# Kernel optimization log

Hardware: AMD Instinct MI355X
Metric: run time of the kernel (lower is better)

Reference implementation:

```python
import jax, jax.numpy as jnp
import numpy as np

B, S, E = 4, 4096, 512

def setup_inputs() -> dict:
    key = jax.random.key(0)
    ks = jax.random.split(key, 9)
    scale = 1.0 / np.sqrt(E)  # keep linear weights at realistic init scale
    return {
        "query": jax.random.normal(ks[0], (B, S, E), jnp.float32),
        "key":   jax.random.normal(ks[1], (B, S, E), jnp.float32),
        "value": jax.random.normal(ks[2], (B, S, E), jnp.float32),
        "Wq": jax.random.normal(ks[3], (E, E), jnp.float32) * scale,
        "bq": jax.random.normal(ks[4], (E,), jnp.float32) * scale,
        "Wk": jax.random.normal(ks[5], (E, E), jnp.float32) * scale,
        "bk": jax.random.normal(ks[6], (E,), jnp.float32) * scale,
        "Wv": jax.random.normal(ks[7], (E, E), jnp.float32) * scale,
        "bv": jax.random.normal(ks[8], (E,), jnp.float32) * scale,
    }

def reference(query, key, value, Wq, bq, Wk, bk, Wv, bv):
    # torch Linear: x @ W^T + b
    q = jnp.einsum('bse,oe->bso', query, Wq) + bq
    k = jnp.einsum('bse,oe->bso', key,   Wk) + bk
    v = jnp.einsum('bse,oe->bso', value, Wv) + bv
    # NOTE: module applies NO 1/sqrt(d) scaling (faithful to source)
    scores = jnp.einsum('bqd,bkd->bqk', q, k)          # [B,S,S] materialized
    attn = jax.nn.softmax(scores, axis=-1)
    # dropout is identity in eval / for deterministic reference
    return jnp.einsum('bqk,bkd->bqd', attn, v)         # [B,S,E]
```

## Files before the change

### kernel.cpp

```cpp
#include <hip/hip_runtime.h>

typedef __attribute__((ext_vector_type(8))) _Float16 f16x8;
typedef __attribute__((ext_vector_type(4))) _Float16 f16x4;
typedef __attribute__((ext_vector_type(4))) float f32x4;

#define NB 4
#define NS 4096
#define NE 512

__device__ __forceinline__ f16x8 cvt2(float4 a, float4 b) {
    f16x8 r;
    r[0] = (_Float16)a.x; r[1] = (_Float16)a.y; r[2] = (_Float16)a.z; r[3] = (_Float16)a.w;
    r[4] = (_Float16)b.x; r[5] = (_Float16)b.y; r[6] = (_Float16)b.z; r[7] = (_Float16)b.w;
    return r;
}
__device__ __forceinline__ void gload_lds16(const void* g, void* l) {
    __builtin_amdgcn_global_load_lds(
        (const __attribute__((address_space(1))) void*)g,
        (__attribute__((address_space(3))) void*)l, 16, 0, 0);
}

__global__ __launch_bounds__(256) void proj_kernel(
    const float* __restrict__ Xq, const float* __restrict__ Xk,
    const float* __restrict__ Xv,
    const float* __restrict__ Wq, const float* __restrict__ Wk,
    const float* __restrict__ Wv,
    const float* __restrict__ bq, const float* __restrict__ bk,
    const float* __restrict__ bv,
    _Float16* __restrict__ oq, _Float16* __restrict__ ok,
    _Float16* __restrict__ ovt, int b0)
{
    __shared__ __align__(16) _Float16 As[128 * 32];
    __shared__ __align__(16) _Float16 Bs[128 * 32];
    const int t = threadIdx.x;
    const int w = t >> 6, ln = t & 63;
    const int which = blockIdx.y;
    const float* X    = (which == 0) ? Xq : ((which == 1) ? Xk : Xv);
    const float* W    = (which == 0) ? Wq : ((which == 1) ? Wk : Wv);
    const float* bias = (which == 0) ? bq : ((which == 1) ? bk : bv);

    const int m0 = (blockIdx.x >> 2) * 128;
    const int n0 = (blockIdx.x & 3) * 128;

    const int srow  = t >> 1;
    const int shalf = (t & 1) * 16;
    const float* gA = X + ((size_t)b0 * NS + m0 + srow) * NE + shalf;
    const float* gB = W + (size_t)(n0 + srow) * NE + shalf;
    _Float16* lA = &As[srow * 32 + shalf];
    _Float16* lB = &Bs[srow * 32 + shalf];

    f32x4 acc[4][4] = {};
    const int wm = (w >> 1) * 64, wn = (w & 1) * 64;
    const int lcol = ln & 15, lq = ln >> 4;

    for (int k0 = 0; k0 < NE; k0 += 32) {
        float4 xa0 = *(const float4*)(gA + k0);
        float4 xa1 = *(const float4*)(gA + k0 + 4);
        float4 xa2 = *(const float4*)(gA + k0 + 8);
        float4 xa3 = *(const float4*)(gA + k0 + 12);
        float4 xb0 = *(const float4*)(gB + k0);
        float4 xb1 = *(const float4*)(gB + k0 + 4);
        float4 xb2 = *(const float4*)(gB + k0 + 8);
        float4 xb3 = *(const float4*)(gB + k0 + 12);
        __syncthreads();
        *(f16x8*)lA       = cvt2(xa0, xa1);
        *(f16x8*)(lA + 8) = cvt2(xa2, xa3);
        *(f16x8*)lB       = cvt2(xb0, xb1);
        *(f16x8*)(lB + 8) = cvt2(xb2, xb3);
        __syncthreads();
        f16x8 a[4], b[4];
#pragma unroll
        for (int i = 0; i < 4; i++)
            a[i] = *(const f16x8*)&As[(wm + i * 16 + lcol) * 32 + lq * 8];
#pragma unroll
        for (int j = 0; j < 4; j++)
            b[j] = *(const f16x8*)&Bs[(wn + j * 16 + lcol) * 32 + lq * 8];
#pragma unroll
        for (int i = 0; i < 4; i++)
#pragma unroll
            for (int j = 0; j < 4; j++)
                acc[i][j] = __builtin_amdgcn_mfma_f32_16x16x32_f16(a[i], b[j], acc[i][j], 0, 0, 0);
    }

    if (which == 0) {
#pragma unroll
        for (int j = 0; j < 4; j++) {
            const int col = n0 + wn + j * 16 + lcol;
            const float bb = bias[col];
#pragma unroll
            for (int i = 0; i < 4; i++) {
                const int rbase = m0 + wm + i * 16 + lq * 4;
#pragma unroll
                for (int r = 0; r < 4; r++)
                    oq[(size_t)(rbase + r) * NE + col] = (_Float16)(acc[i][j][r] + bb);
            }
        }
    } else if (which == 1) {
#pragma unroll
        for (int j = 0; j < 4; j++) {
            const int col = n0 + wn + j * 16 + lcol;
            const int cch = col >> 3, clo = col & 7;
            const float bb = bias[col];
#pragma unroll
            for (int i = 0; i < 4; i++) {
                const int rbase = m0 + wm + i * 16 + lq * 4;
#pragma unroll
                for (int r = 0; r < 4; r++) {
                    const int s = rbase + r;
                    ok[(size_t)s * NE + ((cch ^ (s & 7)) << 3) + clo] =
                        (_Float16)(acc[i][j][r] + bb);
                }
            }
        }
    } else {
#pragma unroll
        for (int j = 0; j < 4; j++) {
            const int d = n0 + wn + j * 16 + lcol;
            const float bb = bias[d];
#pragma unroll
            for (int i = 0; i < 4; i++) {
                const int rbase = m0 + wm + i * 16 + lq * 4;
                const int bat = rbase >> 12;
                const int sl  = rbase & 4095;
                const int kc  = sl >> 6;
                const int slot = ((sl >> 3) & 7) ^ (d & 7);
                f16x4 pk;
#pragma unroll
                for (int r = 0; r < 4; r++) pk[r] = (_Float16)(acc[i][j][r] + bb);
                *(f16x4*)&ovt[(((size_t)bat * 64 + kc) * NE + d) * 64 + slot * 8 + (sl & 7)] = pk;
            }
        }
    }
}

__global__ __launch_bounds__(512, 2) void attn_kernel(
    const _Float16* __restrict__ q, const _Float16* __restrict__ ksw,
    const _Float16* __restrict__ vsw, float* __restrict__ out, int b0)
{
    __shared__ __align__(16) _Float16 Kbuf[64 * 512];
    __shared__ __align__(16) _Float16 Vbuf[512 * 64];
    __shared__ __align__(16) _Float16 Pb[64 * 72];
    __shared__ float mpart[2][64];
    __shared__ float lpart[2][64];

    const int t = threadIdx.x, w = t >> 6, ln = t & 63;
    const int lcol = ln & 15, lq = ln >> 4;
    const int rt = w & 3, g = w >> 2;
    const int xm = lcol & 7;
    const int rel = blockIdx.y, babs = b0 + rel;
    const int q0 = blockIdx.x * 64;

    const _Float16* qp = q + ((size_t)rel * NS + q0 + rt * 16 + lcol) * NE + lq * 8;
    f16x8 qf[16];
#pragma unroll
    for (int ks = 0; ks < 16; ks++) qf[ks] = *(const f16x8*)(qp + ks * 32);

    const _Float16* kbase = ksw + (size_t)rel * NS * NE;
    const _Float16* vbase = vsw + (size_t)rel * NS * NE;

    f32x4 oacc[16] = {};
    float m_st[4] = {-1e30f, -1e30f, -1e30f, -1e30f};
    float l_st[4] = {0.f, 0.f, 0.f, 0.f};

    for (int kc = 0; kc < 64; kc++) {
        __syncthreads();
        const _Float16* kc_src = kbase + (size_t)kc * 64 * NE;
        const _Float16* vc_src = vbase + (size_t)kc * NE * 64;
#pragma unroll
        for (int i = 0; i < 8; i++) {
            const int blk = i * 8 + w;
            gload_lds16(kc_src + (size_t)blk * 512 + ln * 8, (_Float16*)Kbuf + blk * 512);
            gload_lds16(vc_src + (size_t)blk * 512 + ln * 8, (_Float16*)Vbuf + blk * 512);
        }
        __syncthreads();

        f32x4 s0 = {}, s1 = {};
#pragma unroll
        for (int ks = 0; ks < 16; ks++) {
            const int ch = ((ks * 4 + lq) ^ xm) * 8;
            f16x8 kb0 = *(const f16x8*)&Kbuf[(g * 32 + lcol) * 512 + ch];
            f16x8 kb1 = *(const f16x8*)&Kbuf[(g * 32 + 16 + lcol) * 512 + ch];
            s0 = __builtin_amdgcn_mfma_f32_16x16x32_f16(qf[ks], kb0, s0, 0, 0, 0);
            s1 = __builtin_amdgcn_mfma_f32_16x16x32_f16(qf[ks], kb1, s1, 0, 0, 0);
        }
#pragma unroll
        for (int r = 0; r < 4; r++) {
            float vmx = fmaxf(s0[r], s1[r]);
#pragma unroll
            for (int msk = 8; msk; msk >>= 1) vmx = fmaxf(vmx, __shfl_xor(vmx, msk, 64));
            if (lcol == 0) mpart[g][rt * 16 + lq * 4 + r] = vmx;
        }
        __syncthreads();

        float alpha[4];
#pragma unroll
        for (int r = 0; r < 4; r++) {
            const int row = rt * 16 + lq * 4 + r;
            float mc = fmaxf(mpart[0][row], mpart[1][row]);
            float mn = fmaxf(m_st[r], mc);
            alpha[r] = __expf(m_st[r] - mn);
            float p0 = __expf(s0[r] - mn);
            float p1 = __expf(s1[r] - mn);
            Pb[row * 72 + g * 32 + lcol]      = (_Float16)p0;
            Pb[row * 72 + g * 32 + 16 + lcol] = (_Float16)p1;
            float sm = p0 + p1;
#pragma unroll
            for (int msk = 8; msk; msk >>= 1) sm += __shfl_xor(sm, msk, 64);
            if (lcol == 0) lpart[g][row] = sm;
            m_st[r] = mn;
        }
        __syncthreads();
#pragma unroll
        for (int r = 0; r < 4; r++) {
            const int row = rt * 16 + lq * 4 + r;
            l_st[r] = l_st[r] * alpha[r] + lpart[0][row] + lpart[1][row];
        }
        bool allone = (alpha[0] == 1.f) & (alpha[1] == 1.f) &
                      (alpha[2] == 1.f) & (alpha[3] == 1.f);
        if (!__all(allone)) {
#pragma unroll
            for (int et = 0; et < 16; et++) {
                oacc[et][0] *= alpha[0]; oacc[et][1] *= alpha[1];
                oacc[et][2] *= alpha[2]; oacc[et][3] *= alpha[3];
            }
        }
        f16x8 pa0 = *(const f16x8*)&Pb[(rt * 16 + lcol) * 72 + lq * 8];
        f16x8 pa1 = *(const f16x8*)&Pb[(rt * 16 + lcol) * 72 + 32 + lq * 8];
#pragma unroll
        for (int et = 0; et < 16; et++) {
            const int e = g * 256 + et * 16 + lcol;
            f16x8 v0 = *(const f16x8*)&Vbuf[e * 64 + ((lq ^ xm) * 8)];
            f16x8 v1 = *(const f16x8*)&Vbuf[e * 64 + (((4 + lq) ^ xm) * 8)];
            oacc[et] = __builtin_amdgcn_mfma_f32_16x16x32_f16(pa0, v0, oacc[et], 0, 0, 0);
            oacc[et] = __builtin_amdgcn_mfma_f32_16x16x32_f16(pa1, v1, oacc[et], 0, 0, 0);
        }
    }

#pragma unroll
    for (int r = 0; r < 4; r++) {
        const float inv = 1.0f / l_st[r];
        const size_t ob = ((size_t)babs * NS + q0 + rt * 16 + lq * 4 + r) * NE + g * 256 + lcol;
#pragma unroll
        for (int et = 0; et < 16; et++)
            out[ob + et * 16] = oacc[et][r] * inv;
    }
}

extern "C" void kernel_launch(void* const* d_in, const int* in_sizes, int n_in,
                              void* d_out, int out_size, void* d_ws, size_t ws_size,
                              hipStream_t stream) {
    const float* query = (const float*)d_in[0];
    const float* key_  = (const float*)d_in[1];
    const float* value = (const float*)d_in[2];
    const float* Wq    = (const float*)d_in[3];
    const float* bq    = (const float*)d_in[4];
    const float* Wk    = (const float*)d_in[5];
    const float* bk    = (const float*)d_in[6];
    const float* Wv    = (const float*)d_in[7];
    const float* bv    = (const float*)d_in[8];

    const size_t per_batch = (size_t)3 * NS * NE * 2;
    int nb_chunk = (int)(ws_size / per_batch);
    if (nb_chunk > NB) nb_chunk = NB;
    if (nb_chunk < 1)  nb_chunk = 1;

    _Float16* qh  = (_Float16*)d_ws;
    _Float16* kh  = qh + (size_t)nb_chunk * NS * NE;
    _Float16* vth = kh + (size_t)nb_chunk * NS * NE;

    for (int b0 = 0; b0 < NB; b0 += nb_chunk) {
        int nb = NB - b0 < nb_chunk ? NB - b0 : nb_chunk;
        proj_kernel<<<dim3(nb * 128, 3, 1), 256, 0, stream>>>(
            query, key_, value, Wq, Wk, Wv, bq, bk, bv, qh, kh, vth, b0);
        attn_kernel<<<dim3(NS / 64, nb, 1), 512, 0, stream>>>(
            qh, kh, vth, (float*)d_out, b0);
    }
}
```

Before: 518.1 us.

## Double-buffer K/V chunks, halve chunk size, use DPP reductions and prefetch projection loads

The attention kernel now works on 32-key chunks with double-buffered K/V LDS tiles. The next chunk is loaded asynchronously while the current one is computed, and the V layout and swizzle change to match. Row max and row sum reductions use DPP moves instead of shuffles. The projection kernel prefetches the next k-slice into registers and pads its LDS rows to 40 elements to avoid bank conflicts. Smaller chunks mean more iterations and barriers per key, and online-softmax rescaling happens more often.

```diff
diff --git a/kernel.cpp b/kernel.cpp
--- a/kernel.cpp
+++ b/kernel.cpp
@@ -18,6 +18,25 @@
     __builtin_amdgcn_global_load_lds(
         (const __attribute__((address_space(1))) void*)g,
         (__attribute__((address_space(3))) void*)l, 16, 0, 0);
+}
+template <int CTRL>
+__device__ __forceinline__ float dpp_mov(float x) {
+    return __builtin_bit_cast(float,
+        __builtin_amdgcn_mov_dpp(__builtin_bit_cast(int, x), CTRL, 0xF, 0xF, true));
+}
+__device__ __forceinline__ float rowmax16(float v) {
+    v = fmaxf(v, dpp_mov<0x128>(v));
+    v = fmaxf(v, dpp_mov<0x124>(v));
+    v = fmaxf(v, dpp_mov<0x122>(v));
+    v = fmaxf(v, dpp_mov<0x121>(v));
+    return v;
+}
+__device__ __forceinline__ float rowsum16(float v) {
+    v += dpp_mov<0x128>(v);
+    v += dpp_mov<0x124>(v);
+    v += dpp_mov<0x122>(v);
+    v += dpp_mov<0x121>(v);
+    return v;
 }
 
 __global__ __launch_bounds__(256) void proj_kernel(
@@ -30,8 +49,8 @@
     _Float16* __restrict__ oq, _Float16* __restrict__ ok,
     _Float16* __restrict__ ovt, int b0)
 {
-    __shared__ __align__(16) _Float16 As[128 * 32];
-    __shared__ __align__(16) _Float16 Bs[128 * 32];
+    __shared__ __align__(16) _Float16 As[128 * 40];
+    __shared__ __align__(16) _Float16 Bs[128 * 40];
     const int t = threadIdx.x;
     const int w = t >> 6, ln = t & 63;
     const int which = blockIdx.y;
@@ -46,40 +65,46 @@
     const int shalf = (t & 1) * 16;
     const float* gA = X + ((size_t)b0 * NS + m0 + srow) * NE + shalf;
     const float* gB = W + (size_t)(n0 + srow) * NE + shalf;
-    _Float16* lA = &As[srow * 32 + shalf];
-    _Float16* lB = &Bs[srow * 32 + shalf];
+    _Float16* lA = &As[srow * 40 + shalf];
+    _Float16* lB = &Bs[srow * 40 + shalf];
 
     f32x4 acc[4][4] = {};
     const int wm = (w >> 1) * 64, wn = (w & 1) * 64;
     const int lcol = ln & 15, lq = ln >> 4;
 
+    float4 ra0 = *(const float4*)(gA),      ra1 = *(const float4*)(gA + 4);
+    float4 ra2 = *(const float4*)(gA + 8),  ra3 = *(const float4*)(gA + 12);
+    float4 rb0 = *(const float4*)(gB),      rb1 = *(const float4*)(gB + 4);
+    float4 rb2 = *(const float4*)(gB + 8),  rb3 = *(const float4*)(gB + 12);
+
     for (int k0 = 0; k0 < NE; k0 += 32) {
-        float4 xa0 = *(const float4*)(gA + k0);
-        float4 xa1 = *(const float4*)(gA + k0 + 4);
-        float4 xa2 = *(const float4*)(gA + k0 + 8);
-        float4 xa3 = *(const float4*)(gA + k0 + 12);
-        float4 xb0 = *(const float4*)(gB + k0);
-        float4 xb1 = *(const float4*)(gB + k0 + 4);
-        float4 xb2 = *(const float4*)(gB + k0 + 8);
-        float4 xb3 = *(const float4*)(gB + k0 + 12);
-        __syncthreads();
-        *(f16x8*)lA       = cvt2(xa0, xa1);
-        *(f16x8*)(lA + 8) = cvt2(xa2, xa3);
-        *(f16x8*)lB       = cvt2(xb0, xb1);
-        *(f16x8*)(lB + 8) = cvt2(xb2, xb3);
-        __syncthreads();
+        __syncthreads();
+        *(f16x8*)lA       = cvt2(ra0, ra1);
+        *(f16x8*)(lA + 8) = cvt2(ra2, ra3);
+        *(f16x8*)lB       = cvt2(rb0, rb1);
+        *(f16x8*)(lB + 8) = cvt2(rb2, rb3);
+        __syncthreads();
+        const int k1 = (k0 + 32) & (NE - 1);
+        float4 na0 = *(const float4*)(gA + k1),      na1 = *(const float4*)(gA + k1 + 4);
+        float4 na2 = *(const float4*)(gA + k1 + 8),  na3 = *(const float4*)(gA + k1 + 12);
+        float4 nb0 = *(const float4*)(gB + k1),      nb1 = *(const float4*)(gB + k1 + 4);
+        float4 nb2 = *(const float4*)(gB + k1 + 8),  nb3 = *(const float4*)(gB + k1 + 12);
+
         f16x8 a[4], b[4];
 #pragma unroll
         for (int i = 0; i < 4; i++)
-            a[i] = *(const f16x8*)&As[(wm + i * 16 + lcol) * 32 + lq * 8];
+            a[i] = *(const f16x8*)&As[(wm + i * 16 + lcol) * 40 + lq * 8];
 #pragma unroll
         for (int j = 0; j < 4; j++)
-            b[j] = *(const f16x8*)&Bs[(wn + j * 16 + lcol) * 32 + lq * 8];
+            b[j] = *(const f16x8*)&Bs[(wn + j * 16 + lcol) * 40 + lq * 8];
 #pragma unroll
         for (int i = 0; i < 4; i++)
 #pragma unroll
             for (int j = 0; j < 4; j++)
                 acc[i][j] = __builtin_amdgcn_mfma_f32_16x16x32_f16(a[i], b[j], acc[i][j], 0, 0, 0);
+
+        ra0 = na0; ra1 = na1; ra2 = na2; ra3 = na3;
+        rb0 = nb0; rb1 = nb1; rb2 = nb2; rb3 = nb3;
     }
 
     if (which == 0) {
@@ -122,12 +147,12 @@
                 const int rbase = m0 + wm + i * 16 + lq * 4;
                 const int bat = rbase >> 12;
                 const int sl  = rbase & 4095;
-                const int kc  = sl >> 6;
-                const int slot = ((sl >> 3) & 7) ^ (d & 7);
+                const int kc2 = sl >> 5;
+                const int slot = ((sl >> 3) & 3) ^ (d & 3);
                 f16x4 pk;
 #pragma unroll
                 for (int r = 0; r < 4; r++) pk[r] = (_Float16)(acc[i][j][r] + bb);
-                *(f16x4*)&ovt[(((size_t)bat * 64 + kc) * NE + d) * 64 + slot * 8 + (sl & 7)] = pk;
+                *(f16x4*)&ovt[(((size_t)bat * 128 + kc2) * NE + d) * 32 + slot * 8 + (sl & 7)] = pk;
             }
         }
     }
@@ -137,9 +162,9 @@
     const _Float16* __restrict__ q, const _Float16* __restrict__ ksw,
     const _Float16* __restrict__ vsw, float* __restrict__ out, int b0)
 {
-    __shared__ __align__(16) _Float16 Kbuf[64 * 512];
-    __shared__ __align__(16) _Float16 Vbuf[512 * 64];
-    __shared__ __align__(16) _Float16 Pb[64 * 72];
+    __shared__ __align__(16) _Float16 Kbuf[2][32 * 512];
+    __shared__ __align__(16) _Float16 Vbuf[2][512 * 32];
+    __shared__ __align__(16) _Float16 Pb[64 * 40];
     __shared__ float mpart[2][64];
     __shared__ float lpart[2][64];
 
@@ -158,36 +183,40 @@
     const _Float16* kbase = ksw + (size_t)rel * NS * NE;
     const _Float16* vbase = vsw + (size_t)rel * NS * NE;
 
+#pragma unroll
+    for (int i = 0; i < 4; i++) {
+        const int blk = i * 8 + w;
+        gload_lds16(kbase + (size_t)blk * 512 + ln * 8, &Kbuf[0][blk * 512]);
+        gload_lds16(vbase + (size_t)blk * 512 + ln * 8, &Vbuf[0][blk * 512]);
+    }
+
     f32x4 oacc[16] = {};
     float m_st[4] = {-1e30f, -1e30f, -1e30f, -1e30f};
     float l_st[4] = {0.f, 0.f, 0.f, 0.f};
 
-    for (int kc = 0; kc < 64; kc++) {
-        __syncthreads();
-        const _Float16* kc_src = kbase + (size_t)kc * 64 * NE;
-        const _Float16* vc_src = vbase + (size_t)kc * NE * 64;
-#pragma unroll
-        for (int i = 0; i < 8; i++) {
-            const int blk = i * 8 + w;
-            gload_lds16(kc_src + (size_t)blk * 512 + ln * 8, (_Float16*)Kbuf + blk * 512);
-            gload_lds16(vc_src + (size_t)blk * 512 + ln * 8, (_Float16*)Vbuf + blk * 512);
-        }
-        __syncthreads();
-
-        f32x4 s0 = {}, s1 = {};
+    for (int kc = 0; kc < 128; kc++) {
+        const int p = kc & 1;
+        __syncthreads();
+        if (kc + 1 < 128) {
+            const _Float16* kn = kbase + (size_t)(kc + 1) * 32 * 512;
+            const _Float16* vn = vbase + (size_t)(kc + 1) * 512 * 32;
+#pragma unroll
+            for (int i = 0; i < 4; i++) {
+                const int blk = i * 8 + w;
+                gload_lds16(kn + (size_t)blk * 512 + ln * 8, &Kbuf[1 - p][blk * 512]);
+                gload_lds16(vn + (size_t)blk * 512 + ln * 8, &Vbuf[1 - p][blk * 512]);
+            }
+        }
+
+        f32x4 s0 = {};
 #pragma unroll
         for (int ks = 0; ks < 16; ks++) {
-            const int ch = ((ks * 4 + lq) ^ xm) * 8;
-            f16x8 kb0 = *(const f16x8*)&Kbuf[(g * 32 + lcol) * 512 + ch];
-            f16x8 kb1 = *(const f16x8*)&Kbuf[(g * 32 + 16 + lcol) * 512 + ch];
-            s0 = __builtin_amdgcn_mfma_f32_16x16x32_f16(qf[ks], kb0, s0, 0, 0, 0);
-            s1 = __builtin_amdgcn_mfma_f32_16x16x32_f16(qf[ks], kb1, s1, 0, 0, 0);
+            f16x8 kb = *(const f16x8*)&Kbuf[p][(g * 16 + lcol) * 512 + (((ks * 4 + lq) ^ xm) << 3)];
+            s0 = __builtin_amdgcn_mfma_f32_16x16x32_f16(qf[ks], kb, s0, 0, 0, 0);
         }
 #pragma unroll
         for (int r = 0; r < 4; r++) {
-            float vmx = fmaxf(s0[r], s1[r]);
-#pragma unroll
-            for (int msk = 8; msk; msk >>= 1) vmx = fmaxf(vmx, __shfl_xor(vmx, msk, 64));
+            float vmx = rowmax16(s0[r]);
             if (lcol == 0) mpart[g][rt * 16 + lq * 4 + r] = vmx;
         }
         __syncthreads();
@@ -199,13 +228,9 @@
             float mc = fmaxf(mpart[0][row], mpart[1][row]);
             float mn = fmaxf(m_st[r], mc);
             alpha[r] = __expf(m_st[r] - mn);
-            float p0 = __expf(s0[r] - mn);
-            float p1 = __expf(s1[r] - mn);
-            Pb[row * 72 + g * 32 + lcol]      = (_Float16)p0;
-            Pb[row * 72 + g * 32 + 16 + lcol] = (_Float16)p1;
-            float sm = p0 + p1;
-#pragma unroll
-            for (int msk = 8; msk; msk >>= 1) sm += __shfl_xor(sm, msk, 64);
+            float pv = __expf(s0[r] - mn);
+            Pb[row * 40 + g * 16 + lcol] = (_Float16)pv;
+            float sm = rowsum16(pv);
             if (lcol == 0) lpart[g][row] = sm;
             m_st[r] = mn;
         }
@@ -224,15 +249,12 @@
                 oacc[et][2] *= alpha[2]; oacc[et][3] *= alpha[3];
             }
         }
-        f16x8 pa0 = *(const f16x8*)&Pb[(rt * 16 + lcol) * 72 + lq * 8];
-        f16x8 pa1 = *(const f16x8*)&Pb[(rt * 16 + lcol) * 72 + 32 + lq * 8];
+        f16x8 pa = *(const f16x8*)&Pb[(rt * 16 + lcol) * 40 + lq * 8];
 #pragma unroll
         for (int et = 0; et < 16; et++) {
             const int e = g * 256 + et * 16 + lcol;
-            f16x8 v0 = *(const f16x8*)&Vbuf[e * 64 + ((lq ^ xm) * 8)];
-            f16x8 v1 = *(const f16x8*)&Vbuf[e * 64 + (((4 + lq) ^ xm) * 8)];
-            oacc[et] = __builtin_amdgcn_mfma_f32_16x16x32_f16(pa0, v0, oacc[et], 0, 0, 0);
-            oacc[et] = __builtin_amdgcn_mfma_f32_16x16x32_f16(pa1, v1, oacc[et], 0, 0, 0);
+            f16x8 vb = *(const f16x8*)&Vbuf[p][e * 32 + ((lq ^ (e & 3)) << 3)];
+            oacc[et] = __builtin_amdgcn_mfma_f32_16x16x32_f16(pa, vb, oacc[et], 0, 0, 0);
         }
     }
 
```

Result: slower. 529.6 us (+2.2%).
